# Optimization experiments

Measured on AMD Instinct MI355X. Metric: run time of the kernel, lower is better.

The kernel has to match this reference:

```python
import jax, jax.numpy as jnp
import numpy as np

H = W = 256          # render / reference image size (module crops ref to 256x256)
TS = 4               # texture_size in the module
EYE_DIST, ELEV, AZIM = 2.732, 0.0, np.pi / 2  # fixed azimuth (orig: uniform(0,360))
EPS = 1e-8


def _look_at(verts, eye):
    # neural_renderer look_at: at=origin, up=+y
    up = jnp.array([0.0, 1.0, 0.0], dtype=verts.dtype)
    z = -eye / jnp.linalg.norm(eye)
    x = jnp.cross(up, z)
    x = x / jnp.linalg.norm(x)
    y = jnp.cross(z, x)
    R = jnp.stack([x, y, z], axis=0)  # rows = camera axes
    return (verts - eye) @ R.T


def _cross2(u, v):
    return u[..., 0] * v[..., 1] - u[..., 1] * v[..., 0]


def _render(vertices, faces, textures):
    # Orthographic (perspective=False), ambient-only lighting -> color == texture sample.
    eye = jnp.array([EYE_DIST * np.cos(ELEV) * np.sin(AZIM),
                     EYE_DIST * np.sin(ELEV),
                     -EYE_DIST * np.cos(ELEV) * np.cos(AZIM)], dtype=vertices.dtype)
    v = _look_at(vertices[0], eye)            # [V,3] camera space
    fv = v[faces[0]]                          # [F,3,3]
    a, b, c = fv[:, 0, :2], fv[:, 1, :2], fv[:, 2, :2]  # [F,2] screen-space verts
    zf = fv[..., 2]                           # [F,3] per-vertex depth

    # pixel centers in NDC, y flipped (image row 0 = top)
    xs = (jnp.arange(W, dtype=vertices.dtype) + 0.5) / W * 2.0 - 1.0
    ys = 1.0 - (jnp.arange(H, dtype=vertices.dtype) + 0.5) / H * 2.0
    P = jnp.stack(jnp.meshgrid(xs, ys, indexing='xy'), -1).reshape(-1, 2)  # [HW,2]
    Pq = P[:, None, :]                        # [HW,1,2]

    denom = _cross2(b - a, c - a)             # [F] signed 2*area
    w0 = _cross2((c - b)[None], Pq - b[None])  # [HW,F] edge functions
    w1 = _cross2((a - c)[None], Pq - c[None])
    w2 = _cross2((b - a)[None], Pq - a[None])
    s = jnp.sign(denom)[None]
    nondeg = (jnp.abs(denom) > EPS)[None]
    inside = (w0 * s >= 0) & (w1 * s >= 0) & (w2 * s >= 0) & nondeg
    d = jnp.where(jnp.abs(denom) > EPS, denom, 1.0)[None]
    w0, w1, w2 = w0 / d, w1 / d, w2 / d       # normalized barycentrics
    depth = w0 * zf[None, :, 0] + w1 * zf[None, :, 1] + w2 * zf[None, :, 2]  # [HW,F]
    visible = inside & (depth > 0)

    # z-buffer: nearest visible face per pixel
    zbuf = jnp.where(visible, depth, jnp.inf)
    best = jnp.argmin(zbuf, axis=1)           # [HW]
    hit = jnp.take_along_axis(visible, best[:, None], 1)[:, 0]
    bw = jnp.stack([jnp.take_along_axis(wi, best[:, None], 1)[:, 0]
                    for wi in (w0, w1, w2)], axis=-1)  # [HW,3]

    # sample face texture cube [TS,TS,TS] by barycentric coords (nearest)
    ti = jnp.clip(jnp.round(bw * (TS - 1)).astype(jnp.int32), 0, TS - 1)
    color = textures[0][best, ti[:, 0], ti[:, 1], ti[:, 2]]  # [HW,3]
    img = jnp.where(hit[:, None], color, jnp.zeros_like(color)).reshape(H, W, 3)
    return jnp.transpose(img, (2, 0, 1))[None]  # [1,3,H,W]


def setup_inputs() -> dict:
    key = jax.random.key(0)
    k1, k2, k3, k4 = jax.random.split(key, 4)
    V, F = 642, 512
    verts = jax.random.normal(k1, (1, V, 3), jnp.float32)
    verts = verts / (jnp.linalg.norm(verts, axis=-1, keepdims=True) + 1e-6)  # unit sphere
    faces = jax.random.randint(k2, (1, F, 3), 0, V, jnp.int32)
    textures = jax.random.normal(k3, (1, F, TS, TS, TS, 3), jnp.float32)
    image_ref = jax.random.uniform(k4, (1, 3, H, W), jnp.float32)
    return {"vertices": verts, "textures": textures, "image_ref": image_ref, "faces": faces}


def reference(vertices, textures, image_ref, faces):
    image = _render(vertices, faces, jnp.tanh(textures))
    return jnp.sum((image - image_ref) ** 2)
```

## Files before the change

kernel.cpp:

```cpp
#include <hip/hip_runtime.h>
#include <math.h>

#define NFACE 512
#define NVERT 642
#define NPIX  (256 * 256)
#define DXS   (2.0f / 256.0f)

#define EYEX 2.732f
#define EYEZ (-1.6728675276352845e-16f)
#define CC0  (6.123233995736766e-17f)

__global__ __launch_bounds__(256) void render_loss(
    const float* __restrict__ verts,
    const int*   __restrict__ faces,
    const float* __restrict__ tex,
    const float* __restrict__ ref,
    float* __restrict__ out)
{
    __shared__ float  sverts[NVERT * 3];
    __shared__ float4 sf0[NFACE];
    __shared__ float4 sf1[NFACE];
    __shared__ float4 flist[NFACE];
    __shared__ float4 plist[NFACE][3];
    __shared__ int   fcnt, pcnt;
    __shared__ unsigned Mu;
    __shared__ float wsum[4];

    int tid = threadIdx.x;
    if (tid == 0) { fcnt = 0; pcnt = 0; Mu = 0x7f800000u; }

    for (int k = tid; k < NVERT * 3; k += 256) sverts[k] = verts[k];
    __syncthreads();

    int tileX = (blockIdx.x & 15) << 4;
    int tileY = (blockIdx.x >> 4) << 4;
    float xlo = (tileX + 0.5f)  * DXS - 1.0f;
    float xhi = (tileX + 15.5f) * DXS - 1.0f;
    float yhi = 1.0f - (tileY + 0.5f)  * DXS;
    float ylo = 1.0f - (tileY + 15.5f) * DXS;

    float rc[2][9];
    int   rcls[2];
    float rdmn[2];
#pragma unroll
    for (int it = 0; it < 2; ++it) {
        int f = tid + it * 256;
        rcls[it] = 0;
        float vx[3], vy[3], vz[3];
#pragma unroll
        for (int k = 0; k < 3; ++k) {
            int vi = faces[f * 3 + k];
            float px = sverts[vi * 3 + 0];
            float py = sverts[vi * 3 + 1];
            float pz = sverts[vi * 3 + 2];
            float dx = px - EYEX;
            float dz = pz - EYEZ;
            vx[k] = CC0 * dx + dz;
            vy[k] = py;
            vz[k] = -dx + CC0 * dz;
        }
        float ax = vx[0], ay = vy[0];
        float bx = vx[1], by = vy[1];
        float cx = vx[2], cy = vy[2];
        float denom = (bx - ax) * (cy - ay) - (by - ay) * (cx - ax);
        if (fabsf(denom) <= 1e-8f) continue;

        float si = 1.0f / denom;
        float e0x = cx - bx, e0y = cy - by;
        float e1x = ax - cx, e1y = ay - cy;
        float e2x = bx - ax, e2y = by - ay;
        float A0 = e0x * si, B0 = -e0y * si, C0 = (e0y * bx - e0x * by) * si;
        float A1 = e1x * si, B1 = -e1y * si, C1 = (e1y * cx - e1x * cy) * si;
        float A2 = e2x * si, B2 = -e2y * si, C2 = (e2y * ax - e2x * ay) * si;
        float DA = A0 * vz[0] + A1 * vz[1] + A2 * vz[2];
        float DB = B0 * vz[0] + B1 * vz[1] + B2 * vz[2];
        float DC = C0 * vz[0] + C1 * vz[1] + C2 * vz[2];

        sf0[f] = make_float4(A0, B0, C0, A1);
        sf1[f] = make_float4(B1, C1, DA, DB);

        float bxmn = fminf(fminf(ax, bx), cx), bxmx = fmaxf(fmaxf(ax, bx), cx);
        float bymn = fminf(fminf(ay, by), cy), bymx = fmaxf(fmaxf(ay, by), cy);
        if ((bxmn > xhi + 1e-5f) | (bxmx < xlo - 1e-5f) |
            (bymn > yhi + 1e-5f) | (bymx < ylo - 1e-5f)) continue;

        float wmx[3], wmn[3], mg[3];
        float As[3] = {A0, A1, A2}, Bs[3] = {B0, B1, B2}, Cs[3] = {C0, C1, C2};
#pragma unroll
        for (int k = 0; k < 3; ++k) {
            float t1 = As[k] * ylo, t2 = As[k] * yhi;
            float u1 = Bs[k] * xlo, u2 = Bs[k] * xhi;
            wmx[k] = fmaxf(t1, t2) + fmaxf(u1, u2) + Cs[k];
            wmn[k] = fminf(t1, t2) + fminf(u1, u2) + Cs[k];
            mg[k]  = (fabsf(As[k]) + fabsf(Bs[k]) + fabsf(Cs[k])) * 2e-6f;
        }
        if ((wmx[0] < -mg[0]) | (wmx[1] < -mg[1]) | (wmx[2] < -mg[2])) continue;
        bool full = (wmn[0] > mg[0]) & (wmn[1] > mg[1]) & (wmn[2] > mg[2]);

        float t1 = DA * ylo, t2 = DA * yhi;
        float u1 = DB * xlo, u2 = DB * xhi;
        float dmx = fmaxf(t1, t2) + fmaxf(u1, u2) + DC;
        float dmn = fminf(t1, t2) + fminf(u1, u2) + DC;
        float md  = (fabsf(DA) + fabsf(DB) + fabsf(DC)) * 2e-6f + 1e-4f;
        rdmn[it] = dmn - md;
        rcls[it] = full ? 1 : 2;
        rc[it][0] = A0; rc[it][1] = B0; rc[it][2] = C0;
        rc[it][3] = A1; rc[it][4] = B1; rc[it][5] = C1;
        rc[it][6] = DA; rc[it][7] = DB; rc[it][8] = DC;
        if (full) atomicMin(&Mu, __float_as_uint(dmx + md));
    }
    __syncthreads();

    float M = __uint_as_float(Mu);
#pragma unroll
    for (int it = 0; it < 2; ++it) {
        if (rcls[it] == 0 || rdmn[it] > M) continue;
        int f = tid + it * 256;
        float fb = __uint_as_float((unsigned)f);
        if (rcls[it] == 1) {
            int s = atomicAdd(&fcnt, 1);
            flist[s] = make_float4(rc[it][6], rc[it][7], rc[it][8], fb);
        } else {
            int s = atomicAdd(&pcnt, 1);
            plist[s][0] = make_float4(rc[it][0], rc[it][1], rc[it][2], rc[it][3]);
            plist[s][1] = make_float4(rc[it][4], rc[it][5], rc[it][6], rc[it][7]);
            plist[s][2] = make_float4(rc[it][8], fb, 0.f, 0.f);
        }
    }
    __syncthreads();
    int fc = fcnt, pc = pcnt;

    int i = tileX + (tid & 15);
    int j = tileY + (tid >> 4);
    float Px = (i + 0.5f) * DXS - 1.0f;
    float Py = 1.0f - (j + 0.5f) * DXS;

    unsigned best = 0xFFFFFFFFu;
    int k = 0;
    for (; k + 4 <= fc; k += 4) {
        float4 ra = flist[k + 0], rb = flist[k + 1];
        float4 rcc = flist[k + 2], rd = flist[k + 3];
        float da = fmaf(ra.x, Py, fmaf(ra.y, Px, ra.z));
        float db = fmaf(rb.x, Py, fmaf(rb.y, Px, rb.z));
        float dc = fmaf(rcc.x, Py, fmaf(rcc.y, Px, rcc.z));
        float dd = fmaf(rd.x, Py, fmaf(rd.y, Px, rd.z));
        unsigned ca = (__float_as_uint(da) & 0xFFFFFE00u) | __float_as_uint(ra.w);
        unsigned cb = (__float_as_uint(db) & 0xFFFFFE00u) | __float_as_uint(rb.w);
        unsigned cc = (__float_as_uint(dc) & 0xFFFFFE00u) | __float_as_uint(rcc.w);
        unsigned cd = (__float_as_uint(dd) & 0xFFFFFE00u) | __float_as_uint(rd.w);
        ca = ca < cb ? ca : cb;
        cc = cc < cd ? cc : cd;
        ca = ca < cc ? ca : cc;
        best = best < ca ? best : ca;
    }
    for (; k < fc; ++k) {
        float4 r = flist[k];
        float dep = fmaf(r.x, Py, fmaf(r.y, Px, r.z));
        unsigned cand = (__float_as_uint(dep) & 0xFFFFFE00u) | __float_as_uint(r.w);
        best = best < cand ? best : cand;
    }
    k = 0;
    for (; k + 2 <= pc; k += 2) {
        float4 a0 = plist[k][0], a1 = plist[k][1], a2 = plist[k][2];
        float4 b0 = plist[k+1][0], b1 = plist[k+1][1], b2 = plist[k+1][2];
        float aw0 = fmaf(a0.x, Py, fmaf(a0.y, Px, a0.z));
        float aw1 = fmaf(a0.w, Py, fmaf(a1.x, Px, a1.y));
        float aw2 = 1.0f - aw0 - aw1;
        float adp = fmaf(a1.z, Py, fmaf(a1.w, Px, a2.x));
        float amn = fminf(fminf(aw0, aw1), aw2);
        unsigned ac = (__float_as_uint(adp) & 0xFFFFFE00u) | __float_as_uint(a2.y);
        ac = (amn >= 0.f) ? ac : 0xFFFFFFFFu;
        float bw0 = fmaf(b0.x, Py, fmaf(b0.y, Px, b0.z));
        float bw1 = fmaf(b0.w, Py, fmaf(b1.x, Px, b1.y));
        float bw2 = 1.0f - bw0 - bw1;
        float bdp = fmaf(b1.z, Py, fmaf(b1.w, Px, b2.x));
        float bmn = fminf(fminf(bw0, bw1), bw2);
        unsigned bc = (__float_as_uint(bdp) & 0xFFFFFE00u) | __float_as_uint(b2.y);
        bc = (bmn >= 0.f) ? bc : 0xFFFFFFFFu;
        ac = ac < bc ? ac : bc;
        best = best < ac ? best : ac;
    }
    for (; k < pc; ++k) {
        float4 q0 = plist[k][0], q1 = plist[k][1], q2 = plist[k][2];
        float w0  = fmaf(q0.x, Py, fmaf(q0.y, Px, q0.z));
        float w1  = fmaf(q0.w, Py, fmaf(q1.x, Px, q1.y));
        float w2  = 1.0f - w0 - w1;
        float dep = fmaf(q1.z, Py, fmaf(q1.w, Px, q2.x));
        float mn  = fminf(fminf(w0, w1), w2);
        unsigned cand = (__float_as_uint(dep) & 0xFFFFFE00u) | __float_as_uint(q2.y);
        cand = (mn >= 0.f) ? cand : 0xFFFFFFFFu;
        best = best < cand ? best : cand;
    }

    int p = j * 256 + i;
    float col0 = 0.f, col1 = 0.f, col2 = 0.f;
    if (best != 0xFFFFFFFFu) {
        int bf = (int)(best & 511u);
        float4 q0 = sf0[bf];
        float4 q1 = sf1[bf];
        float w0 = fmaf(q0.x, Py, fmaf(q0.y, Px, q0.z));
        float w1 = fmaf(q0.w, Py, fmaf(q1.x, Px, q1.y));
        float w2 = 1.0f - w0 - w1;
        int t0 = (int)rintf(w0 * 3.0f); t0 = t0 < 0 ? 0 : (t0 > 3 ? 3 : t0);
        int t1 = (int)rintf(w1 * 3.0f); t1 = t1 < 0 ? 0 : (t1 > 3 ? 3 : t1);
        int t2 = (int)rintf(w2 * 3.0f); t2 = t2 < 0 ? 0 : (t2 > 3 ? 3 : t2);
        const float* tp = tex + ((((bf * 4 + t0) * 4 + t1) * 4 + t2) * 3);
        col0 = tanhf(tp[0]);
        col1 = tanhf(tp[1]);
        col2 = tanhf(tp[2]);
    }
    float r0 = ref[0 * NPIX + p];
    float r1 = ref[1 * NPIX + p];
    float r2 = ref[2 * NPIX + p];
    float e0 = col0 - r0, e1 = col1 - r1, e2 = col2 - r2;
    float loss = e0 * e0 + e1 * e1 + e2 * e2;

    for (int off = 32; off > 0; off >>= 1)
        loss += __shfl_down(loss, off, 64);
    int lane = tid & 63;
    int wid  = tid >> 6;
    if (lane == 0) wsum[wid] = loss;
    __syncthreads();
    if (tid == 0)
        atomicAdd(out, wsum[0] + wsum[1] + wsum[2] + wsum[3]);
}

extern "C" void kernel_launch(void* const* d_in, const int* in_sizes, int n_in,
                              void* d_out, int out_size, void* d_ws, size_t ws_size,
                              hipStream_t stream) {
    const float* verts = (const float*)d_in[0];
    const float* tex   = (const float*)d_in[1];
    const float* ref   = (const float*)d_in[2];
    const int*   faces = (const int*)d_in[3];
    float* out = (float*)d_out;

    hipMemsetAsync(out, 0, sizeof(float), stream);
    render_loss<<<256, 256, 0, stream>>>(verts, faces, tex, ref, out);
}
```

Baseline: 17.67 us.

## Split face setup into separate kernel and render with 8x8 single-wave tiles

Per-face transform and edge-equation setup moves out of the render kernel into a small pre-pass that writes face records to workspace, so tiles stop redundantly recomputing all 512 faces. The render kernel now uses 1024 blocks of 64 threads (8x8 pixel tiles) that read precomputed records and bounding boxes from global memory. A finalize kernel reduces the per-block sums in place of the memset plus atomic. This adds two extra kernel launches and more global reads of face data per tile, traded against removing duplicated setup math and getting more blocks for occupancy.

Result: slower. 23.15 us (+31.0%).

```diff
diff --git a/kernel.cpp b/kernel.cpp
--- a/kernel.cpp
+++ b/kernel.cpp
@@ -10,128 +10,150 @@
 #define EYEZ (-1.6728675276352845e-16f)
 #define CC0  (6.123233995736766e-17f)
 
-__global__ __launch_bounds__(256) void render_loss(
+__global__ __launch_bounds__(256) void setup_faces(
     const float* __restrict__ verts,
     const int*   __restrict__ faces,
+    float* __restrict__ ws)
+{
+    int f = blockIdx.x * 256 + threadIdx.x;
+    if (f >= NFACE) return;
+    float4* tb0 = (float4*)ws;
+    float4* tb1 = tb0 + NFACE;
+    float4* tb2 = tb0 + 2 * NFACE;
+    float4* tb3 = tb0 + 3 * NFACE;
+
+    float vx[3], vy[3], vz[3];
+#pragma unroll
+    for (int k = 0; k < 3; ++k) {
+        int vi = faces[f * 3 + k];
+        float px = verts[vi * 3 + 0];
+        float py = verts[vi * 3 + 1];
+        float pz = verts[vi * 3 + 2];
+        float dx = px - EYEX;
+        float dz = pz - EYEZ;
+        vx[k] = CC0 * dx + dz;
+        vy[k] = py;
+        vz[k] = -dx + CC0 * dz;
+    }
+    float ax = vx[0], ay = vy[0];
+    float bx = vx[1], by = vy[1];
+    float cx = vx[2], cy = vy[2];
+    float denom = (bx - ax) * (cy - ay) - (by - ay) * (cx - ax);
+    if (fabsf(denom) <= 1e-8f) {
+        tb0[f] = make_float4(0.f, 0.f, 0.f, 0.f);
+        tb1[f] = make_float4(0.f, 0.f, 0.f, 0.f);
+        tb2[f] = make_float4(0.f, 3e30f, -3e30f, 3e30f);
+        tb3[f] = make_float4(-3e30f, 0.f, 0.f, 0.f);
+        return;
+    }
+    float si = 1.0f / denom;
+    float e0x = cx - bx, e0y = cy - by;
+    float e1x = ax - cx, e1y = ay - cy;
+    float A0 = e0x * si, B0 = -e0y * si, C0 = (e0y * bx - e0x * by) * si;
+    float A1 = e1x * si, B1 = -e1y * si, C1 = (e1y * cx - e1x * cy) * si;
+    float A2 = -(A0 + A1), B2 = -(B0 + B1), C2 = 1.0f - C0 - C1;
+    float DA = A0 * vz[0] + A1 * vz[1] + A2 * vz[2];
+    float DB = B0 * vz[0] + B1 * vz[1] + B2 * vz[2];
+    float DC = C0 * vz[0] + C1 * vz[1] + C2 * vz[2];
+    float xmn = fminf(fminf(ax, bx), cx), xmx = fmaxf(fmaxf(ax, bx), cx);
+    float ymn = fminf(fminf(ay, by), cy), ymx = fmaxf(fmaxf(ay, by), cy);
+
+    tb0[f] = make_float4(A0, B0, C0, A1);
+    tb1[f] = make_float4(B1, C1, DA, DB);
+    tb2[f] = make_float4(DC, xmn, xmx, ymn);
+    tb3[f] = make_float4(ymx, 0.f, 0.f, 0.f);
+}
+
+__global__ __launch_bounds__(64) void render_tile(
+    const float4* __restrict__ tb,
     const float* __restrict__ tex,
     const float* __restrict__ ref,
-    float* __restrict__ out)
+    float* __restrict__ bsum)
 {
-    __shared__ float  sverts[NVERT * 3];
-    __shared__ float4 sf0[NFACE];
-    __shared__ float4 sf1[NFACE];
     __shared__ float4 flist[NFACE];
     __shared__ float4 plist[NFACE][3];
-    __shared__ int   fcnt, pcnt;
+    __shared__ int fcnt, pcnt;
     __shared__ unsigned Mu;
-    __shared__ float wsum[4];
-
-    int tid = threadIdx.x;
-    if (tid == 0) { fcnt = 0; pcnt = 0; Mu = 0x7f800000u; }
-
-    for (int k = tid; k < NVERT * 3; k += 256) sverts[k] = verts[k];
-    __syncthreads();
-
-    int tileX = (blockIdx.x & 15) << 4;
-    int tileY = (blockIdx.x >> 4) << 4;
-    float xlo = (tileX + 0.5f)  * DXS - 1.0f;
-    float xhi = (tileX + 15.5f) * DXS - 1.0f;
-    float yhi = 1.0f - (tileY + 0.5f)  * DXS;
-    float ylo = 1.0f - (tileY + 15.5f) * DXS;
-
-    float rc[2][9];
-    int   rcls[2];
-    float rdmn[2];
-#pragma unroll
-    for (int it = 0; it < 2; ++it) {
-        int f = tid + it * 256;
-        rcls[it] = 0;
-        float vx[3], vy[3], vz[3];
+
+    const float4* tb0 = tb;
+    const float4* tb1 = tb + NFACE;
+    const float4* tb2 = tb + 2 * NFACE;
+    const float4* tb3 = tb + 3 * NFACE;
+
+    int lane = threadIdx.x;
+    if (lane == 0) { fcnt = 0; pcnt = 0; Mu = 0x7f800000u; }
+    __syncthreads();
+
+    int tileX = (blockIdx.x & 31) << 3;
+    int tileY = (blockIdx.x >> 5) << 3;
+    float xlo = (tileX + 0.5f) * DXS - 1.0f;
+    float xhi = (tileX + 7.5f) * DXS - 1.0f;
+    float yhi = 1.0f - (tileY + 0.5f) * DXS;
+    float ylo = 1.0f - (tileY + 7.5f) * DXS;
+
+    int   rcls[8];
+    float rdmn[8];
+#pragma unroll
+    for (int r = 0; r < 8; ++r) {
+        int f = r * 64 + lane;
+        rcls[r] = 0;
+        float4 q2 = tb2[f];
+        float4 q3 = tb3[f];
+        if ((q2.y > xhi + 1e-5f) | (q2.z < xlo - 1e-5f) |
+            (q2.w > yhi + 1e-5f) | (q3.x < ylo - 1e-5f)) continue;
+        float4 q0 = tb0[f];
+        float4 q1 = tb1[f];
+        float A0 = q0.x, B0 = q0.y, C0 = q0.z, A1 = q0.w, B1 = q1.x, C1 = q1.y;
+        float DA = q1.z, DB = q1.w, DC = q2.x;
+        float A2 = -(A0 + A1), B2 = -(B0 + B1), C2 = 1.0f - C0 - C1;
+        float As[3] = {A0, A1, A2}, Bs[3] = {B0, B1, B2}, Cs[3] = {C0, C1, C2};
+        bool rej = false, full = true;
 #pragma unroll
         for (int k = 0; k < 3; ++k) {
-            int vi = faces[f * 3 + k];
-            float px = sverts[vi * 3 + 0];
-            float py = sverts[vi * 3 + 1];
-            float pz = sverts[vi * 3 + 2];
-            float dx = px - EYEX;
-            float dz = pz - EYEZ;
-            vx[k] = CC0 * dx + dz;
-            vy[k] = py;
-            vz[k] = -dx + CC0 * dz;
+            float ta = As[k] * ylo, tb_ = As[k] * yhi;
+            float ua = Bs[k] * xlo, ub = Bs[k] * xhi;
+            float wmx = fmaxf(ta, tb_) + fmaxf(ua, ub) + Cs[k];
+            float wmn = fminf(ta, tb_) + fminf(ua, ub) + Cs[k];
+            float mg  = (fabsf(As[k]) + fabsf(Bs[k]) + fabsf(Cs[k])) * 2e-6f;
+            rej  = rej  | (wmx < -mg);
+            full = full & (wmn > mg);
         }
-        float ax = vx[0], ay = vy[0];
-        float bx = vx[1], by = vy[1];
-        float cx = vx[2], cy = vy[2];
-        float denom = (bx - ax) * (cy - ay) - (by - ay) * (cx - ax);
-        if (fabsf(denom) <= 1e-8f) continue;
-
-        float si = 1.0f / denom;
-        float e0x = cx - bx, e0y = cy - by;
-        float e1x = ax - cx, e1y = ay - cy;
-        float e2x = bx - ax, e2y = by - ay;
-        float A0 = e0x * si, B0 = -e0y * si, C0 = (e0y * bx - e0x * by) * si;
-        float A1 = e1x * si, B1 = -e1y * si, C1 = (e1y * cx - e1x * cy) * si;
-        float A2 = e2x * si, B2 = -e2y * si, C2 = (e2y * ax - e2x * ay) * si;
-        float DA = A0 * vz[0] + A1 * vz[1] + A2 * vz[2];
-        float DB = B0 * vz[0] + B1 * vz[1] + B2 * vz[2];
-        float DC = C0 * vz[0] + C1 * vz[1] + C2 * vz[2];
-
-        sf0[f] = make_float4(A0, B0, C0, A1);
-        sf1[f] = make_float4(B1, C1, DA, DB);
-
-        float bxmn = fminf(fminf(ax, bx), cx), bxmx = fmaxf(fmaxf(ax, bx), cx);
-        float bymn = fminf(fminf(ay, by), cy), bymx = fmaxf(fmaxf(ay, by), cy);
-        if ((bxmn > xhi + 1e-5f) | (bxmx < xlo - 1e-5f) |
-            (bymn > yhi + 1e-5f) | (bymx < ylo - 1e-5f)) continue;
-
-        float wmx[3], wmn[3], mg[3];
-        float As[3] = {A0, A1, A2}, Bs[3] = {B0, B1, B2}, Cs[3] = {C0, C1, C2};
-#pragma unroll
-        for (int k = 0; k < 3; ++k) {
-            float t1 = As[k] * ylo, t2 = As[k] * yhi;
-            float u1 = Bs[k] * xlo, u2 = Bs[k] * xhi;
-            wmx[k] = fmaxf(t1, t2) + fmaxf(u1, u2) + Cs[k];
-            wmn[k] = fminf(t1, t2) + fminf(u1, u2) + Cs[k];
-            mg[k]  = (fabsf(As[k]) + fabsf(Bs[k]) + fabsf(Cs[k])) * 2e-6f;
-        }
-        if ((wmx[0] < -mg[0]) | (wmx[1] < -mg[1]) | (wmx[2] < -mg[2])) continue;
-        bool full = (wmn[0] > mg[0]) & (wmn[1] > mg[1]) & (wmn[2] > mg[2]);
-
-        float t1 = DA * ylo, t2 = DA * yhi;
-        float u1 = DB * xlo, u2 = DB * xhi;
-        float dmx = fmaxf(t1, t2) + fmaxf(u1, u2) + DC;
-        float dmn = fminf(t1, t2) + fminf(u1, u2) + DC;
+        if (rej) continue;
+        float da = DA * ylo, db = DA * yhi;
+        float ea = DB * xlo, eb = DB * xhi;
+        float dmx = fmaxf(da, db) + fmaxf(ea, eb) + DC;
+        float dmn = fminf(da, db) + fminf(ea, eb) + DC;
         float md  = (fabsf(DA) + fabsf(DB) + fabsf(DC)) * 2e-6f + 1e-4f;
-        rdmn[it] = dmn - md;
-        rcls[it] = full ? 1 : 2;
-        rc[it][0] = A0; rc[it][1] = B0; rc[it][2] = C0;
-        rc[it][3] = A1; rc[it][4] = B1; rc[it][5] = C1;
-        rc[it][6] = DA; rc[it][7] = DB; rc[it][8] = DC;
+        rdmn[r] = dmn - md;
+        rcls[r] = full ? 1 : 2;
         if (full) atomicMin(&Mu, __float_as_uint(dmx + md));
     }
     __syncthreads();
-
     float M = __uint_as_float(Mu);
-#pragma unroll
-    for (int it = 0; it < 2; ++it) {
-        if (rcls[it] == 0 || rdmn[it] > M) continue;
-        int f = tid + it * 256;
+
+#pragma unroll
+    for (int r = 0; r < 8; ++r) {
+        if (rcls[r] == 0 || rdmn[r] > M) continue;
+        int f = r * 64 + lane;
+        float4 q0 = tb0[f];
+        float4 q1 = tb1[f];
+        float4 q2 = tb2[f];
         float fb = __uint_as_float((unsigned)f);
-        if (rcls[it] == 1) {
+        if (rcls[r] == 1) {
             int s = atomicAdd(&fcnt, 1);
-            flist[s] = make_float4(rc[it][6], rc[it][7], rc[it][8], fb);
+            flist[s] = make_float4(q1.z, q1.w, q2.x, fb);
         } else {
             int s = atomicAdd(&pcnt, 1);
-            plist[s][0] = make_float4(rc[it][0], rc[it][1], rc[it][2], rc[it][3]);
-            plist[s][1] = make_float4(rc[it][4], rc[it][5], rc[it][6], rc[it][7]);
-            plist[s][2] = make_float4(rc[it][8], fb, 0.f, 0.f);
+            plist[s][0] = q0;
+            plist[s][1] = q1;
+            plist[s][2] = make_float4(q2.x, fb, 0.f, 0.f);
         }
     }
     __syncthreads();
     int fc = fcnt, pc = pcnt;
 
-    int i = tileX + (tid & 15);
-    int j = tileY + (tid >> 4);
+    int i = tileX + (lane & 7);
+    int j = tileY + (lane >> 3);
     float Px = (i + 0.5f) * DXS - 1.0f;
     float Py = 1.0f - (j + 0.5f) * DXS;
 
@@ -139,14 +161,14 @@
     int k = 0;
     for (; k + 4 <= fc; k += 4) {
         float4 ra = flist[k + 0], rb = flist[k + 1];
-        float4 rcc = flist[k + 2], rd = flist[k + 3];
+        float4 rc = flist[k + 2], rd = flist[k + 3];
         float da = fmaf(ra.x, Py, fmaf(ra.y, Px, ra.z));
         float db = fmaf(rb.x, Py, fmaf(rb.y, Px, rb.z));
-        float dc = fmaf(rcc.x, Py, fmaf(rcc.y, Px, rcc.z));
+        float dc = fmaf(rc.x, Py, fmaf(rc.y, Px, rc.z));
         float dd = fmaf(rd.x, Py, fmaf(rd.y, Px, rd.z));
         unsigned ca = (__float_as_uint(da) & 0xFFFFFE00u) | __float_as_uint(ra.w);
         unsigned cb = (__float_as_uint(db) & 0xFFFFFE00u) | __float_as_uint(rb.w);
-        unsigned cc = (__float_as_uint(dc) & 0xFFFFFE00u) | __float_as_uint(rcc.w);
+        unsigned cc = (__float_as_uint(dc) & 0xFFFFFE00u) | __float_as_uint(rc.w);
         unsigned cd = (__float_as_uint(dd) & 0xFFFFFE00u) | __float_as_uint(rd.w);
         ca = ca < cb ? ca : cb;
         cc = cc < cd ? cc : cd;
@@ -196,8 +218,8 @@
     float col0 = 0.f, col1 = 0.f, col2 = 0.f;
     if (best != 0xFFFFFFFFu) {
         int bf = (int)(best & 511u);
-        float4 q0 = sf0[bf];
-        float4 q1 = sf1[bf];
+        float4 q0 = tb0[bf];
+        float4 q1 = tb1[bf];
         float w0 = fmaf(q0.x, Py, fmaf(q0.y, Px, q0.z));
         float w1 = fmaf(q0.w, Py, fmaf(q1.x, Px, q1.y));
         float w2 = 1.0f - w0 - w1;
@@ -217,12 +239,23 @@
 
     for (int off = 32; off > 0; off >>= 1)
         loss += __shfl_down(loss, off, 64);
+    if (lane == 0) bsum[blockIdx.x] = loss;
+}
+
+__global__ __launch_bounds__(256) void finalize(
+    const float* __restrict__ bsum,
+    float* __restrict__ out)
+{
+    __shared__ float wsum[4];
+    int tid = threadIdx.x;
+    float v = bsum[tid] + bsum[tid + 256] + bsum[tid + 512] + bsum[tid + 768];
+    for (int off = 32; off > 0; off >>= 1)
+        v += __shfl_down(v, off, 64);
     int lane = tid & 63;
     int wid  = tid >> 6;
-    if (lane == 0) wsum[wid] = loss;
-    __syncthreads();
-    if (tid == 0)
-        atomicAdd(out, wsum[0] + wsum[1] + wsum[2] + wsum[3]);
+    if (lane == 0) wsum[wid] = v;
+    __syncthreads();
+    if (tid == 0) out[0] = wsum[0] + wsum[1] + wsum[2] + wsum[3];
 }
 
 extern "C" void kernel_launch(void* const* d_in, const int* in_sizes, int n_in,
@@ -233,7 +266,9 @@
     const float* ref   = (const float*)d_in[2];
     const int*   faces = (const int*)d_in[3];
     float* out = (float*)d_out;
-
-    hipMemsetAsync(out, 0, sizeof(float), stream);
-    render_loss<<<256, 256, 0, stream>>>(verts, faces, tex, ref, out);
-}
+    float* ws  = (float*)d_ws;
+
+    setup_faces<<<2, 256, 0, stream>>>(verts, faces, ws);
+    render_tile<<<1024, 64, 0, stream>>>((const float4*)ws, tex, ref, ws + 8192);
+    finalize<<<1, 256, 0, stream>>>(ws + 8192, out);
+}
```

## Bin faces per 8x8 sub-tile with ballot-built index lists

Applied to the files above, without the earlier changes.

Each 16x16 tile is split into four 8x8 quadrants, each owned by one wavefront. Faces are classified, and occlusion-culled by depth bound, per quadrant, so each wave tests fewer faces. The shared face lists are built with ballot masks and popcount prefix sums instead of atomic counters, and they store indices into the per-face coefficient arrays rather than copied coefficients. This adds per-face classification work and an extra indirection on each shared-memory load, and the quadrant layout changes the pixel mapping.

Result: slower. 21.45 us (+21.4%).

```diff
diff --git a/kernel.cpp b/kernel.cpp
--- a/kernel.cpp
+++ b/kernel.cpp
@@ -20,14 +20,16 @@
     __shared__ float  sverts[NVERT * 3];
     __shared__ float4 sf0[NFACE];
     __shared__ float4 sf1[NFACE];
-    __shared__ float4 flist[NFACE];
-    __shared__ float4 plist[NFACE][3];
-    __shared__ int   fcnt, pcnt;
-    __shared__ unsigned Mu;
+    __shared__ float4 sdep[NFACE];
+    __shared__ unsigned long long fmask[4][8], pmask[4][8];
+    __shared__ unsigned Mu[4];
+    __shared__ unsigned fidx[4][NFACE], pidx[4][NFACE];
     __shared__ float wsum[4];
 
-    int tid = threadIdx.x;
-    if (tid == 0) { fcnt = 0; pcnt = 0; Mu = 0x7f800000u; }
+    int tid  = threadIdx.x;
+    int lane = tid & 63;
+    int w    = tid >> 6;
+    if (tid < 4) Mu[tid] = 0x7f800000u;
 
     for (int k = tid; k < NVERT * 3; k += 256) sverts[k] = verts[k];
     __syncthreads();
@@ -38,14 +40,16 @@
     float xhi = (tileX + 15.5f) * DXS - 1.0f;
     float yhi = 1.0f - (tileY + 0.5f)  * DXS;
     float ylo = 1.0f - (tileY + 15.5f) * DXS;
-
-    float rc[2][9];
-    int   rcls[2];
-    float rdmn[2];
+    float xcm = 0.5f * (xlo + xhi);
+    float ycm = 0.5f * (ylo + yhi);
+    const float H  = 3.5f * DXS;
+    const float Q  = 4.0f * DXS;
+
+    unsigned cls = 0;
+    float dmn8[8];
 #pragma unroll
     for (int it = 0; it < 2; ++it) {
         int f = tid + it * 256;
-        rcls[it] = 0;
         float vx[3], vy[3], vz[3];
 #pragma unroll
         for (int k = 0; k < 3; ++k) {
@@ -63,90 +67,110 @@
         float bx = vx[1], by = vy[1];
         float cx = vx[2], cy = vy[2];
         float denom = (bx - ax) * (cy - ay) - (by - ay) * (cx - ax);
-        if (fabsf(denom) <= 1e-8f) continue;
-
-        float si = 1.0f / denom;
+        bool ok = fabsf(denom) > 1e-8f;
+        float si = ok ? (1.0f / denom) : 0.0f;
         float e0x = cx - bx, e0y = cy - by;
         float e1x = ax - cx, e1y = ay - cy;
-        float e2x = bx - ax, e2y = by - ay;
         float A0 = e0x * si, B0 = -e0y * si, C0 = (e0y * bx - e0x * by) * si;
         float A1 = e1x * si, B1 = -e1y * si, C1 = (e1y * cx - e1x * cy) * si;
-        float A2 = e2x * si, B2 = -e2y * si, C2 = (e2y * ax - e2x * ay) * si;
+        float A2 = -(A0 + A1), B2 = -(B0 + B1), C2 = 1.0f - C0 - C1;
         float DA = A0 * vz[0] + A1 * vz[1] + A2 * vz[2];
         float DB = B0 * vz[0] + B1 * vz[1] + B2 * vz[2];
         float DC = C0 * vz[0] + C1 * vz[1] + C2 * vz[2];
-
-        sf0[f] = make_float4(A0, B0, C0, A1);
-        sf1[f] = make_float4(B1, C1, DA, DB);
+        sf0[f]  = make_float4(A0, B0, C0, A1);
+        sf1[f]  = make_float4(B1, C1, DA, DB);
+        sdep[f] = make_float4(DA, DB, DC, __uint_as_float((unsigned)f));
+        if (!ok) continue;
 
         float bxmn = fminf(fminf(ax, bx), cx), bxmx = fmaxf(fmaxf(ax, bx), cx);
         float bymn = fminf(fminf(ay, by), cy), bymx = fmaxf(fmaxf(ay, by), cy);
         if ((bxmn > xhi + 1e-5f) | (bxmx < xlo - 1e-5f) |
             (bymn > yhi + 1e-5f) | (bymx < ylo - 1e-5f)) continue;
 
-        float wmx[3], wmn[3], mg[3];
         float As[3] = {A0, A1, A2}, Bs[3] = {B0, B1, B2}, Cs[3] = {C0, C1, C2};
+        float wc[3], Aq[3], Bq[3], ee[3], mg[3];
 #pragma unroll
         for (int k = 0; k < 3; ++k) {
-            float t1 = As[k] * ylo, t2 = As[k] * yhi;
-            float u1 = Bs[k] * xlo, u2 = Bs[k] * xhi;
-            wmx[k] = fmaxf(t1, t2) + fmaxf(u1, u2) + Cs[k];
-            wmn[k] = fminf(t1, t2) + fminf(u1, u2) + Cs[k];
-            mg[k]  = (fabsf(As[k]) + fabsf(Bs[k]) + fabsf(Cs[k])) * 2e-6f;
-        }
-        if ((wmx[0] < -mg[0]) | (wmx[1] < -mg[1]) | (wmx[2] < -mg[2])) continue;
-        bool full = (wmn[0] > mg[0]) & (wmn[1] > mg[1]) & (wmn[2] > mg[2]);
-
-        float t1 = DA * ylo, t2 = DA * yhi;
-        float u1 = DB * xlo, u2 = DB * xhi;
-        float dmx = fmaxf(t1, t2) + fmaxf(u1, u2) + DC;
-        float dmn = fminf(t1, t2) + fminf(u1, u2) + DC;
-        float md  = (fabsf(DA) + fabsf(DB) + fabsf(DC)) * 2e-6f + 1e-4f;
-        rdmn[it] = dmn - md;
-        rcls[it] = full ? 1 : 2;
-        rc[it][0] = A0; rc[it][1] = B0; rc[it][2] = C0;
-        rc[it][3] = A1; rc[it][4] = B1; rc[it][5] = C1;
-        rc[it][6] = DA; rc[it][7] = DB; rc[it][8] = DC;
-        if (full) atomicMin(&Mu, __float_as_uint(dmx + md));
-    }
-    __syncthreads();
-
-    float M = __uint_as_float(Mu);
+            wc[k] = fmaf(As[k], ycm, fmaf(Bs[k], xcm, Cs[k]));
+            Aq[k] = As[k] * Q;
+            Bq[k] = Bs[k] * Q;
+            ee[k] = (fabsf(As[k]) + fabsf(Bs[k])) * H;
+            mg[k] = (fabsf(As[k]) + fabsf(Bs[k]) + fabsf(Cs[k])) * 4e-6f;
+        }
+        float dc  = fmaf(DA, ycm, fmaf(DB, xcm, DC));
+        float DAq = DA * Q, DBq = DB * Q;
+        float de  = (fabsf(DA) + fabsf(DB)) * H;
+        float md  = (fabsf(DA) + fabsf(DB) + fabsf(DC)) * 4e-6f + 1e-4f;
+
+#pragma unroll
+        for (int s = 0; s < 4; ++s) {
+            float fx = (s & 1) ? 1.0f : -1.0f;
+            float fy = (s & 2) ? -1.0f : 1.0f;
+            bool rej = false, full = true;
+#pragma unroll
+            for (int k = 0; k < 3; ++k) {
+                float wcs = wc[k] + fy * Aq[k] + fx * Bq[k];
+                rej  = rej  | (wcs + ee[k] < -mg[k]);
+                full = full & (wcs - ee[k] >  mg[k]);
+            }
+            if (rej) continue;
+            float dcs = dc + fy * DAq + fx * DBq;
+            dmn8[it * 4 + s] = dcs - de - md;
+            cls |= (full ? 1u : 2u) << (2 * (it * 4 + s));
+            if (full) atomicMin(&Mu[s], __float_as_uint(dcs + de + md));
+        }
+    }
+    __syncthreads();
+
+    float Ms0 = __uint_as_float(Mu[0]), Ms1 = __uint_as_float(Mu[1]);
+    float Ms2 = __uint_as_float(Mu[2]), Ms3 = __uint_as_float(Mu[3]);
+    float Ms[4] = {Ms0, Ms1, Ms2, Ms3};
 #pragma unroll
     for (int it = 0; it < 2; ++it) {
-        if (rcls[it] == 0 || rdmn[it] > M) continue;
-        int f = tid + it * 256;
-        float fb = __uint_as_float((unsigned)f);
-        if (rcls[it] == 1) {
-            int s = atomicAdd(&fcnt, 1);
-            flist[s] = make_float4(rc[it][6], rc[it][7], rc[it][8], fb);
-        } else {
-            int s = atomicAdd(&pcnt, 1);
-            plist[s][0] = make_float4(rc[it][0], rc[it][1], rc[it][2], rc[it][3]);
-            plist[s][1] = make_float4(rc[it][4], rc[it][5], rc[it][6], rc[it][7]);
-            plist[s][2] = make_float4(rc[it][8], fb, 0.f, 0.f);
-        }
-    }
-    __syncthreads();
-    int fc = fcnt, pc = pcnt;
-
-    int i = tileX + (tid & 15);
-    int j = tileY + (tid >> 4);
+#pragma unroll
+        for (int s = 0; s < 4; ++s) {
+            unsigned c = (cls >> (2 * (it * 4 + s))) & 3u;
+            bool alive = (c != 0u) && (dmn8[it * 4 + s] <= Ms[s]);
+            unsigned long long bf = __ballot(alive && (c == 1u));
+            unsigned long long bp = __ballot(alive && (c == 2u));
+            if (lane == 0) {
+                fmask[s][it * 4 + w] = bf;
+                pmask[s][it * 4 + w] = bp;
+            }
+        }
+    }
+    __syncthreads();
+
+    unsigned long long ltm = (1ull << lane) - 1ull;
+    int fc = 0, pc = 0;
+#pragma unroll
+    for (int jj = 0; jj < 8; ++jj) {
+        unsigned long long m = fmask[w][jj];
+        if ((m >> lane) & 1ull) fidx[w][fc + (int)__popcll(m & ltm)] = jj * 64 + lane;
+        fc += (int)__popcll(m);
+        m = pmask[w][jj];
+        if ((m >> lane) & 1ull) pidx[w][pc + (int)__popcll(m & ltm)] = jj * 64 + lane;
+        pc += (int)__popcll(m);
+    }
+
+    int i = tileX + ((w & 1) << 3) + (lane & 7);
+    int j = tileY + ((w >> 1) << 3) + (lane >> 3);
     float Px = (i + 0.5f) * DXS - 1.0f;
     float Py = 1.0f - (j + 0.5f) * DXS;
 
     unsigned best = 0xFFFFFFFFu;
     int k = 0;
     for (; k + 4 <= fc; k += 4) {
-        float4 ra = flist[k + 0], rb = flist[k + 1];
-        float4 rcc = flist[k + 2], rd = flist[k + 3];
+        uint4 id = *(const uint4*)&fidx[w][k];
+        float4 ra = sdep[id.x], rb = sdep[id.y];
+        float4 rc = sdep[id.z], rd = sdep[id.w];
         float da = fmaf(ra.x, Py, fmaf(ra.y, Px, ra.z));
         float db = fmaf(rb.x, Py, fmaf(rb.y, Px, rb.z));
-        float dc = fmaf(rcc.x, Py, fmaf(rcc.y, Px, rcc.z));
+        float dc = fmaf(rc.x, Py, fmaf(rc.y, Px, rc.z));
         float dd = fmaf(rd.x, Py, fmaf(rd.y, Px, rd.z));
         unsigned ca = (__float_as_uint(da) & 0xFFFFFE00u) | __float_as_uint(ra.w);
         unsigned cb = (__float_as_uint(db) & 0xFFFFFE00u) | __float_as_uint(rb.w);
-        unsigned cc = (__float_as_uint(dc) & 0xFFFFFE00u) | __float_as_uint(rcc.w);
+        unsigned cc = (__float_as_uint(dc) & 0xFFFFFE00u) | __float_as_uint(rc.w);
         unsigned cd = (__float_as_uint(dd) & 0xFFFFFE00u) | __float_as_uint(rd.w);
         ca = ca < cb ? ca : cb;
         cc = cc < cd ? cc : cd;
@@ -154,40 +178,42 @@
         best = best < ca ? best : ca;
     }
     for (; k < fc; ++k) {
-        float4 r = flist[k];
+        float4 r = sdep[fidx[w][k]];
         float dep = fmaf(r.x, Py, fmaf(r.y, Px, r.z));
         unsigned cand = (__float_as_uint(dep) & 0xFFFFFE00u) | __float_as_uint(r.w);
         best = best < cand ? best : cand;
     }
     k = 0;
     for (; k + 2 <= pc; k += 2) {
-        float4 a0 = plist[k][0], a1 = plist[k][1], a2 = plist[k][2];
-        float4 b0 = plist[k+1][0], b1 = plist[k+1][1], b2 = plist[k+1][2];
+        uint2 id = *(const uint2*)&pidx[w][k];
+        float4 a0 = sf0[id.x], a1 = sf1[id.x], a2 = sdep[id.x];
+        float4 b0 = sf0[id.y], b1 = sf1[id.y], b2 = sdep[id.y];
         float aw0 = fmaf(a0.x, Py, fmaf(a0.y, Px, a0.z));
         float aw1 = fmaf(a0.w, Py, fmaf(a1.x, Px, a1.y));
         float aw2 = 1.0f - aw0 - aw1;
-        float adp = fmaf(a1.z, Py, fmaf(a1.w, Px, a2.x));
+        float adp = fmaf(a2.x, Py, fmaf(a2.y, Px, a2.z));
         float amn = fminf(fminf(aw0, aw1), aw2);
-        unsigned ac = (__float_as_uint(adp) & 0xFFFFFE00u) | __float_as_uint(a2.y);
+        unsigned ac = (__float_as_uint(adp) & 0xFFFFFE00u) | __float_as_uint(a2.w);
         ac = (amn >= 0.f) ? ac : 0xFFFFFFFFu;
         float bw0 = fmaf(b0.x, Py, fmaf(b0.y, Px, b0.z));
         float bw1 = fmaf(b0.w, Py, fmaf(b1.x, Px, b1.y));
         float bw2 = 1.0f - bw0 - bw1;
-        float bdp = fmaf(b1.z, Py, fmaf(b1.w, Px, b2.x));
+        float bdp = fmaf(b2.x, Py, fmaf(b2.y, Px, b2.z));
         float bmn = fminf(fminf(bw0, bw1), bw2);
-        unsigned bc = (__float_as_uint(bdp) & 0xFFFFFE00u) | __float_as_uint(b2.y);
+        unsigned bc = (__float_as_uint(bdp) & 0xFFFFFE00u) | __float_as_uint(b2.w);
         bc = (bmn >= 0.f) ? bc : 0xFFFFFFFFu;
         ac = ac < bc ? ac : bc;
         best = best < ac ? best : ac;
     }
     for (; k < pc; ++k) {
-        float4 q0 = plist[k][0], q1 = plist[k][1], q2 = plist[k][2];
+        unsigned idx = pidx[w][k];
+        float4 q0 = sf0[idx], q1 = sf1[idx], q2 = sdep[idx];
         float w0  = fmaf(q0.x, Py, fmaf(q0.y, Px, q0.z));
         float w1  = fmaf(q0.w, Py, fmaf(q1.x, Px, q1.y));
         float w2  = 1.0f - w0 - w1;
-        float dep = fmaf(q1.z, Py, fmaf(q1.w, Px, q2.x));
+        float dep = fmaf(q2.x, Py, fmaf(q2.y, Px, q2.z));
         float mn  = fminf(fminf(w0, w1), w2);
-        unsigned cand = (__float_as_uint(dep) & 0xFFFFFE00u) | __float_as_uint(q2.y);
+        unsigned cand = (__float_as_uint(dep) & 0xFFFFFE00u) | __float_as_uint(q2.w);
         cand = (mn >= 0.f) ? cand : 0xFFFFFFFFu;
         best = best < cand ? best : cand;
     }
@@ -217,9 +243,7 @@
 
     for (int off = 32; off > 0; off >>= 1)
         loss += __shfl_down(loss, off, 64);
-    int lane = tid & 63;
-    int wid  = tid >> 6;
-    if (lane == 0) wsum[wid] = loss;
+    if (lane == 0) wsum[w] = loss;
     __syncthreads();
     if (tid == 0)
         atomicAdd(out, wsum[0] + wsum[1] + wsum[2] + wsum[3]);
```

## Split tiles into half-tile face lists and use cooperative grid reduction

Applied to the files above, without the earlier changes.

Each 16x16 tile is split into two 8-row halves, and each half gets its own full/partial face list and depth cull bound, so each wavefront tests fewer faces. Shared storage is restructured into packed p0/p1/pd arrays, with full faces stored from the top end, and the winning face's barycentric coefficients are recomputed from the vertices instead of being cached. The memset and atomicAdd on the output are replaced by a cooperative launch with a grid sync and a deterministic final sum in block 0. Grid sync and cooperative-launch overhead may offset the culling gains.

New measurement: 65.80 us. 272% more time.

```diff
diff --git a/kernel.cpp b/kernel.cpp
--- a/kernel.cpp
+++ b/kernel.cpp
@@ -1,5 +1,8 @@
 #include <hip/hip_runtime.h>
+#include <hip/hip_cooperative_groups.h>
 #include <math.h>
+
+namespace cg = cooperative_groups;
 
 #define NFACE 512
 #define NVERT 642
@@ -15,19 +18,21 @@
     const int*   __restrict__ faces,
     const float* __restrict__ tex,
     const float* __restrict__ ref,
+    float* __restrict__ bsum,
     float* __restrict__ out)
 {
     __shared__ float  sverts[NVERT * 3];
-    __shared__ float4 sf0[NFACE];
-    __shared__ float4 sf1[NFACE];
-    __shared__ float4 flist[NFACE];
-    __shared__ float4 plist[NFACE][3];
-    __shared__ int   fcnt, pcnt;
-    __shared__ unsigned Mu;
+    __shared__ float4 p0[2][NFACE];
+    __shared__ float4 p1[2][NFACE];
+    __shared__ float2 pd[2][NFACE];
+    __shared__ int fcnt[2], pcnt[2];
+    __shared__ unsigned Mu[2];
     __shared__ float wsum[4];
 
-    int tid = threadIdx.x;
-    if (tid == 0) { fcnt = 0; pcnt = 0; Mu = 0x7f800000u; }
+    int tid  = threadIdx.x;
+    int lane = tid & 63;
+    int w    = tid >> 6;
+    if (tid < 2) { fcnt[tid] = 0; pcnt[tid] = 0; Mu[tid] = 0x7f800000u; }
 
     for (int k = tid; k < NVERT * 3; k += 256) sverts[k] = verts[k];
     __syncthreads();
@@ -36,16 +41,19 @@
     int tileY = (blockIdx.x >> 4) << 4;
     float xlo = (tileX + 0.5f)  * DXS - 1.0f;
     float xhi = (tileX + 15.5f) * DXS - 1.0f;
-    float yhi = 1.0f - (tileY + 0.5f)  * DXS;
-    float ylo = 1.0f - (tileY + 15.5f) * DXS;
+    float yhis[2], ylos[2];
+    yhis[0] = 1.0f - (tileY + 0.5f)  * DXS;
+    ylos[0] = 1.0f - (tileY + 7.5f)  * DXS;
+    yhis[1] = 1.0f - (tileY + 8.5f)  * DXS;
+    ylos[1] = 1.0f - (tileY + 15.5f) * DXS;
+    float tylo = ylos[1], tyhi = yhis[0];
 
     float rc[2][9];
-    int   rcls[2];
-    float rdmn[2];
+    float rdm[2][2];
+    unsigned cls = 0;
 #pragma unroll
     for (int it = 0; it < 2; ++it) {
         int f = tid + it * 256;
-        rcls[it] = 0;
         float vx[3], vy[3], vz[3];
 #pragma unroll
         for (int k = 0; k < 3; ++k) {
@@ -68,85 +76,99 @@
         float si = 1.0f / denom;
         float e0x = cx - bx, e0y = cy - by;
         float e1x = ax - cx, e1y = ay - cy;
-        float e2x = bx - ax, e2y = by - ay;
         float A0 = e0x * si, B0 = -e0y * si, C0 = (e0y * bx - e0x * by) * si;
         float A1 = e1x * si, B1 = -e1y * si, C1 = (e1y * cx - e1x * cy) * si;
-        float A2 = e2x * si, B2 = -e2y * si, C2 = (e2y * ax - e2x * ay) * si;
+        float A2 = -(A0 + A1), B2 = -(B0 + B1), C2 = 1.0f - C0 - C1;
         float DA = A0 * vz[0] + A1 * vz[1] + A2 * vz[2];
         float DB = B0 * vz[0] + B1 * vz[1] + B2 * vz[2];
         float DC = C0 * vz[0] + C1 * vz[1] + C2 * vz[2];
-
-        sf0[f] = make_float4(A0, B0, C0, A1);
-        sf1[f] = make_float4(B1, C1, DA, DB);
-
-        float bxmn = fminf(fminf(ax, bx), cx), bxmx = fmaxf(fmaxf(ax, bx), cx);
-        float bymn = fminf(fminf(ay, by), cy), bymx = fmaxf(fmaxf(ay, by), cy);
-        if ((bxmn > xhi + 1e-5f) | (bxmx < xlo - 1e-5f) |
-            (bymn > yhi + 1e-5f) | (bymx < ylo - 1e-5f)) continue;
-
-        float wmx[3], wmn[3], mg[3];
-        float As[3] = {A0, A1, A2}, Bs[3] = {B0, B1, B2}, Cs[3] = {C0, C1, C2};
-#pragma unroll
-        for (int k = 0; k < 3; ++k) {
-            float t1 = As[k] * ylo, t2 = As[k] * yhi;
-            float u1 = Bs[k] * xlo, u2 = Bs[k] * xhi;
-            wmx[k] = fmaxf(t1, t2) + fmaxf(u1, u2) + Cs[k];
-            wmn[k] = fminf(t1, t2) + fminf(u1, u2) + Cs[k];
-            mg[k]  = (fabsf(As[k]) + fabsf(Bs[k]) + fabsf(Cs[k])) * 2e-6f;
-        }
-        if ((wmx[0] < -mg[0]) | (wmx[1] < -mg[1]) | (wmx[2] < -mg[2])) continue;
-        bool full = (wmn[0] > mg[0]) & (wmn[1] > mg[1]) & (wmn[2] > mg[2]);
-
-        float t1 = DA * ylo, t2 = DA * yhi;
-        float u1 = DB * xlo, u2 = DB * xhi;
-        float dmx = fmaxf(t1, t2) + fmaxf(u1, u2) + DC;
-        float dmn = fminf(t1, t2) + fminf(u1, u2) + DC;
-        float md  = (fabsf(DA) + fabsf(DB) + fabsf(DC)) * 2e-6f + 1e-4f;
-        rdmn[it] = dmn - md;
-        rcls[it] = full ? 1 : 2;
         rc[it][0] = A0; rc[it][1] = B0; rc[it][2] = C0;
         rc[it][3] = A1; rc[it][4] = B1; rc[it][5] = C1;
         rc[it][6] = DA; rc[it][7] = DB; rc[it][8] = DC;
-        if (full) atomicMin(&Mu, __float_as_uint(dmx + md));
-    }
-    __syncthreads();
-
-    float M = __uint_as_float(Mu);
+
+        float bxmn = fminf(fminf(ax, bx), cx), bxmx = fmaxf(fmaxf(ax, bx), cx);
+        float bymn = fminf(fminf(ay, by), cy), bymx = fmaxf(fmaxf(ay, by), cy);
+        if ((bxmn > xhi + 1e-5f) | (bxmx < tylo - 1e-5f) |
+            (bymn > tyhi + 1e-5f) | (bymx < tylo - 1e-5f) |
+            (bxmx < xlo - 1e-5f) | (bymn > tyhi + 1e-5f)) {  }
+        if ((bxmn > xhi + 1e-5f) | (bxmx < xlo - 1e-5f) |
+            (bymn > tyhi + 1e-5f) | (bymx < tylo - 1e-5f)) continue;
+
+        float As[3] = {A0, A1, A2}, Bs[3] = {B0, B1, B2}, Cs[3] = {C0, C1, C2};
+        float bmx[3], bmn[3], mg[3];
+#pragma unroll
+        for (int k = 0; k < 3; ++k) {
+            float u1 = Bs[k] * xlo, u2 = Bs[k] * xhi;
+            bmx[k] = fmaxf(u1, u2);
+            bmn[k] = fminf(u1, u2);
+            mg[k]  = (fabsf(As[k]) + fabsf(Bs[k]) + fabsf(Cs[k])) * 4e-6f;
+        }
+        float dbx = fmaxf(DB * xlo, DB * xhi);
+        float dbn = fminf(DB * xlo, DB * xhi);
+        float md  = (fabsf(DA) + fabsf(DB) + fabsf(DC)) * 4e-6f + 1e-4f;
+
+#pragma unroll
+        for (int h = 0; h < 2; ++h) {
+            bool rej = false, full = true;
+#pragma unroll
+            for (int k = 0; k < 3; ++k) {
+                float t1 = As[k] * ylos[h], t2 = As[k] * yhis[h];
+                float wmx = fmaxf(t1, t2) + bmx[k] + Cs[k];
+                float wmn = fminf(t1, t2) + bmn[k] + Cs[k];
+                rej  = rej  | (wmx < -mg[k]);
+                full = full & (wmn >  mg[k]);
+            }
+            if (rej) continue;
+            float t1 = DA * ylos[h], t2 = DA * yhis[h];
+            float dmx = fmaxf(t1, t2) + dbx + DC;
+            float dmn = fminf(t1, t2) + dbn + DC;
+            rdm[it][h] = dmn - md;
+            cls |= (full ? 1u : 2u) << (2 * (it * 2 + h));
+            if (full) atomicMin(&Mu[h], __float_as_uint(dmx + md));
+        }
+    }
+    __syncthreads();
+
+    float Mh[2] = { __uint_as_float(Mu[0]), __uint_as_float(Mu[1]) };
 #pragma unroll
     for (int it = 0; it < 2; ++it) {
-        if (rcls[it] == 0 || rdmn[it] > M) continue;
-        int f = tid + it * 256;
-        float fb = __uint_as_float((unsigned)f);
-        if (rcls[it] == 1) {
-            int s = atomicAdd(&fcnt, 1);
-            flist[s] = make_float4(rc[it][6], rc[it][7], rc[it][8], fb);
-        } else {
-            int s = atomicAdd(&pcnt, 1);
-            plist[s][0] = make_float4(rc[it][0], rc[it][1], rc[it][2], rc[it][3]);
-            plist[s][1] = make_float4(rc[it][4], rc[it][5], rc[it][6], rc[it][7]);
-            plist[s][2] = make_float4(rc[it][8], fb, 0.f, 0.f);
-        }
-    }
-    __syncthreads();
-    int fc = fcnt, pc = pcnt;
-
-    int i = tileX + (tid & 15);
-    int j = tileY + (tid >> 4);
+        float fidf = __uint_as_float((unsigned)(tid + it * 256));
+#pragma unroll
+        for (int h = 0; h < 2; ++h) {
+            unsigned c = (cls >> (2 * (it * 2 + h))) & 3u;
+            if (c == 0u || rdm[it][h] > Mh[h]) continue;
+            if (c == 1u) {
+                int s = atomicAdd(&fcnt[h], 1);
+                p0[h][511 - s] = make_float4(rc[it][6], rc[it][7], rc[it][8], fidf);
+            } else {
+                int s = atomicAdd(&pcnt[h], 1);
+                p0[h][s] = make_float4(rc[it][0], rc[it][1], rc[it][2], rc[it][3]);
+                p1[h][s] = make_float4(rc[it][4], rc[it][5], rc[it][6], rc[it][7]);
+                pd[h][s] = make_float2(rc[it][8], fidf);
+            }
+        }
+    }
+    __syncthreads();
+
+    int h  = w >> 1;
+    int fc = fcnt[h], pc = pcnt[h];
+    int i = tileX + ((w & 1) << 3) + (lane & 7);
+    int j = tileY + (h << 3) + (lane >> 3);
     float Px = (i + 0.5f) * DXS - 1.0f;
     float Py = 1.0f - (j + 0.5f) * DXS;
 
     unsigned best = 0xFFFFFFFFu;
     int k = 0;
     for (; k + 4 <= fc; k += 4) {
-        float4 ra = flist[k + 0], rb = flist[k + 1];
-        float4 rcc = flist[k + 2], rd = flist[k + 3];
+        float4 ra = p0[h][511 - k], rb = p0[h][510 - k];
+        float4 rc4 = p0[h][509 - k], rd = p0[h][508 - k];
         float da = fmaf(ra.x, Py, fmaf(ra.y, Px, ra.z));
         float db = fmaf(rb.x, Py, fmaf(rb.y, Px, rb.z));
-        float dc = fmaf(rcc.x, Py, fmaf(rcc.y, Px, rcc.z));
+        float dc = fmaf(rc4.x, Py, fmaf(rc4.y, Px, rc4.z));
         float dd = fmaf(rd.x, Py, fmaf(rd.y, Px, rd.z));
         unsigned ca = (__float_as_uint(da) & 0xFFFFFE00u) | __float_as_uint(ra.w);
         unsigned cb = (__float_as_uint(db) & 0xFFFFFE00u) | __float_as_uint(rb.w);
-        unsigned cc = (__float_as_uint(dc) & 0xFFFFFE00u) | __float_as_uint(rcc.w);
+        unsigned cc = (__float_as_uint(dc) & 0xFFFFFE00u) | __float_as_uint(rc4.w);
         unsigned cd = (__float_as_uint(dd) & 0xFFFFFE00u) | __float_as_uint(rd.w);
         ca = ca < cb ? ca : cb;
         cc = cc < cd ? cc : cd;
@@ -154,40 +176,43 @@
         best = best < ca ? best : ca;
     }
     for (; k < fc; ++k) {
-        float4 r = flist[k];
+        float4 r = p0[h][511 - k];
         float dep = fmaf(r.x, Py, fmaf(r.y, Px, r.z));
         unsigned cand = (__float_as_uint(dep) & 0xFFFFFE00u) | __float_as_uint(r.w);
         best = best < cand ? best : cand;
     }
     k = 0;
     for (; k + 2 <= pc; k += 2) {
-        float4 a0 = plist[k][0], a1 = plist[k][1], a2 = plist[k][2];
-        float4 b0 = plist[k+1][0], b1 = plist[k+1][1], b2 = plist[k+1][2];
+        float4 a0 = p0[h][k], a1 = p1[h][k];
+        float2 ad = pd[h][k];
+        float4 b0 = p0[h][k + 1], b1 = p1[h][k + 1];
+        float2 bd = pd[h][k + 1];
         float aw0 = fmaf(a0.x, Py, fmaf(a0.y, Px, a0.z));
         float aw1 = fmaf(a0.w, Py, fmaf(a1.x, Px, a1.y));
         float aw2 = 1.0f - aw0 - aw1;
-        float adp = fmaf(a1.z, Py, fmaf(a1.w, Px, a2.x));
+        float adp = fmaf(a1.z, Py, fmaf(a1.w, Px, ad.x));
         float amn = fminf(fminf(aw0, aw1), aw2);
-        unsigned ac = (__float_as_uint(adp) & 0xFFFFFE00u) | __float_as_uint(a2.y);
+        unsigned ac = (__float_as_uint(adp) & 0xFFFFFE00u) | __float_as_uint(ad.y);
         ac = (amn >= 0.f) ? ac : 0xFFFFFFFFu;
         float bw0 = fmaf(b0.x, Py, fmaf(b0.y, Px, b0.z));
         float bw1 = fmaf(b0.w, Py, fmaf(b1.x, Px, b1.y));
         float bw2 = 1.0f - bw0 - bw1;
-        float bdp = fmaf(b1.z, Py, fmaf(b1.w, Px, b2.x));
+        float bdp = fmaf(b1.z, Py, fmaf(b1.w, Px, bd.x));
         float bmn = fminf(fminf(bw0, bw1), bw2);
-        unsigned bc = (__float_as_uint(bdp) & 0xFFFFFE00u) | __float_as_uint(b2.y);
+        unsigned bc = (__float_as_uint(bdp) & 0xFFFFFE00u) | __float_as_uint(bd.y);
         bc = (bmn >= 0.f) ? bc : 0xFFFFFFFFu;
         ac = ac < bc ? ac : bc;
         best = best < ac ? best : ac;
     }
     for (; k < pc; ++k) {
-        float4 q0 = plist[k][0], q1 = plist[k][1], q2 = plist[k][2];
+        float4 q0 = p0[h][k], q1 = p1[h][k];
+        float2 qd = pd[h][k];
         float w0  = fmaf(q0.x, Py, fmaf(q0.y, Px, q0.z));
         float w1  = fmaf(q0.w, Py, fmaf(q1.x, Px, q1.y));
         float w2  = 1.0f - w0 - w1;
-        float dep = fmaf(q1.z, Py, fmaf(q1.w, Px, q2.x));
+        float dep = fmaf(q1.z, Py, fmaf(q1.w, Px, qd.x));
         float mn  = fminf(fminf(w0, w1), w2);
-        unsigned cand = (__float_as_uint(dep) & 0xFFFFFE00u) | __float_as_uint(q2.y);
+        unsigned cand = (__float_as_uint(dep) & 0xFFFFFE00u) | __float_as_uint(qd.y);
         cand = (mn >= 0.f) ? cand : 0xFFFFFFFFu;
         best = best < cand ? best : cand;
     }
@@ -196,10 +221,30 @@
     float col0 = 0.f, col1 = 0.f, col2 = 0.f;
     if (best != 0xFFFFFFFFu) {
         int bf = (int)(best & 511u);
-        float4 q0 = sf0[bf];
-        float4 q1 = sf1[bf];
-        float w0 = fmaf(q0.x, Py, fmaf(q0.y, Px, q0.z));
-        float w1 = fmaf(q0.w, Py, fmaf(q1.x, Px, q1.y));
+        float vx[3], vy[3], vz_;
+#pragma unroll
+        for (int kk = 0; kk < 3; ++kk) {
+            int vi = faces[bf * 3 + kk];
+            float px = sverts[vi * 3 + 0];
+            float py = sverts[vi * 3 + 1];
+            float pz = sverts[vi * 3 + 2];
+            float dx = px - EYEX;
+            float dz = pz - EYEZ;
+            vx[kk] = CC0 * dx + dz;
+            vy[kk] = py;
+        }
+        (void)vz_;
+        float ax = vx[0], ay = vy[0];
+        float bx = vx[1], by = vy[1];
+        float cx = vx[2], cy = vy[2];
+        float denom = (bx - ax) * (cy - ay) - (by - ay) * (cx - ax);
+        float si = 1.0f / denom;
+        float e0x = cx - bx, e0y = cy - by;
+        float e1x = ax - cx, e1y = ay - cy;
+        float A0 = e0x * si, B0 = -e0y * si, C0 = (e0y * bx - e0x * by) * si;
+        float A1 = e1x * si, B1 = -e1y * si, C1 = (e1y * cx - e1x * cy) * si;
+        float w0 = fmaf(A0, Py, fmaf(B0, Px, C0));
+        float w1 = fmaf(A1, Py, fmaf(B1, Px, C1));
         float w2 = 1.0f - w0 - w1;
         int t0 = (int)rintf(w0 * 3.0f); t0 = t0 < 0 ? 0 : (t0 > 3 ? 3 : t0);
         int t1 = (int)rintf(w1 * 3.0f); t1 = t1 < 0 ? 0 : (t1 > 3 ? 3 : t1);
@@ -217,12 +262,22 @@
 
     for (int off = 32; off > 0; off >>= 1)
         loss += __shfl_down(loss, off, 64);
-    int lane = tid & 63;
-    int wid  = tid >> 6;
-    if (lane == 0) wsum[wid] = loss;
+    if (lane == 0) wsum[w] = loss;
     __syncthreads();
     if (tid == 0)
-        atomicAdd(out, wsum[0] + wsum[1] + wsum[2] + wsum[3]);
+        bsum[blockIdx.x] = wsum[0] + wsum[1] + wsum[2] + wsum[3];
+    __threadfence();
+
+    cg::this_grid().sync();
+
+    if (blockIdx.x == 0) {
+        float v = bsum[tid];
+        for (int off = 32; off > 0; off >>= 1)
+            v += __shfl_down(v, off, 64);
+        if (lane == 0) wsum[w] = v;
+        __syncthreads();
+        if (tid == 0) out[0] = wsum[0] + wsum[1] + wsum[2] + wsum[3];
+    }
 }
 
 extern "C" void kernel_launch(void* const* d_in, const int* in_sizes, int n_in,
@@ -232,8 +287,11 @@
     const float* tex   = (const float*)d_in[1];
     const float* ref   = (const float*)d_in[2];
     const int*   faces = (const int*)d_in[3];
-    float* out = (float*)d_out;
-
-    hipMemsetAsync(out, 0, sizeof(float), stream);
-    render_loss<<<256, 256, 0, stream>>>(verts, faces, tex, ref, out);
+    float* out  = (float*)d_out;
+    float* bsum = (float*)d_ws;
+
+    void* args[] = { (void*)&verts, (void*)&faces, (void*)&tex, (void*)&ref,
+                     (void*)&bsum, (void*)&out };
+    hipLaunchCooperativeKernel((const void*)render_loss, dim3(256), dim3(256),
+                               args, 0, stream);
 }
```
